# Performance work log

Hardware: AMD Instinct MI355X
Metric: run time of the kernel (lower is better)

Reference implementation:

```python
import jax, jax.numpy as jnp
import numpy as np

N_NODES = 25000
N_EDGES = 250000
DIM = 64
HEADS = 4
BN_EPS = 1e-5


def setup_inputs() -> dict:
    key = jax.random.key(0)
    ks = jax.random.split(key, 6)
    x = jax.random.normal(ks[0], (N_NODES, DIM), dtype=jnp.float32)
    edge_index = jax.random.randint(ks[1], (2, N_EDGES), 0, N_NODES)
    edge_attr = jax.random.normal(ks[2], (N_EDGES, DIM), dtype=jnp.float32)
    # learned params of GATGNN_AGAT_LAYER (xavier-ish scale)
    W = jax.random.normal(ks[3], (2 * DIM, HEADS * DIM), dtype=jnp.float32) * 0.05
    att = jax.random.normal(ks[4], (1, HEADS, 2 * DIM), dtype=jnp.float32) * 0.05
    bias = jnp.zeros((DIM,), dtype=jnp.float32)
    # BatchNorm1d(heads) in eval mode (running stats)
    bn_gamma = jnp.ones((HEADS,), dtype=jnp.float32)
    bn_beta = jnp.zeros((HEADS,), dtype=jnp.float32)
    bn_mean = jnp.zeros((HEADS,), dtype=jnp.float32)
    bn_var = jnp.ones((HEADS,), dtype=jnp.float32)
    return {"x": x, "edge_attr": edge_attr, "W": W, "att": att, "bias": bias,
            "bn_gamma": bn_gamma, "bn_beta": bn_beta, "bn_mean": bn_mean,
            "bn_var": bn_var, "edge_index": edge_index}


def reference(x, edge_attr, W, att, bias, bn_gamma, bn_beta, bn_mean, bn_var, edge_index):
    act = jax.nn.softplus  # act='softplus' in DSDCrystal
    # flow='target_to_source': i = edge_index[0] (aggregation index), j = edge_index[1]
    idx_i = edge_index[0]
    idx_j = edge_index[1]
    x_i = x[idx_i]                                   # [E, D] gather
    x_j = x[idx_j]                                   # [E, D] gather
    out_i = act(jnp.concatenate([x_i, edge_attr], axis=-1) @ W)  # [E, H*D]
    out_j = act(jnp.concatenate([x_j, edge_attr], axis=-1) @ W)  # [E, H*D]
    out_i = out_i.reshape(-1, HEADS, DIM)            # [E, H, D]
    out_j = out_j.reshape(-1, HEADS, DIM)
    # multi-head attention logits
    alpha = act(jnp.sum(jnp.concatenate([out_i, out_j], axis=-1) * att, axis=-1))  # [E, H]
    # BatchNorm1d(heads), eval mode
    alpha = act((alpha - bn_mean) / jnp.sqrt(bn_var + BN_EPS) * bn_gamma + bn_beta)
    # segment softmax over edges sharing the same target node i
    amax = jax.ops.segment_max(alpha, idx_i, num_segments=N_NODES)  # [N, H]
    e = jnp.exp(alpha - amax[idx_i])
    denom = jax.ops.segment_sum(e, idx_i, num_segments=N_NODES)[idx_i]  # [E, H]
    alpha = e / denom
    # weighted messages, scatter-add aggregation (dropout p=0.0 / eval)
    msg = out_j * alpha[:, :, None]                  # [E, H, D]
    aggr = jax.ops.segment_sum(msg, idx_i, num_segments=N_NODES)  # [N, H, D]
    # update: mean over heads + bias
    return aggr.mean(axis=1) + bias                  # [N, D]
```

## Files before the change

kernel.cpp:

```cpp
#include <hip/hip_runtime.h>
#include <hip/hip_bf16.h>
#include <math.h>

#define NN 25000
#define NE 250000
#define DD 64
#define HH 4
#define NGROUP (NE / 16)
#define NB 98

typedef __attribute__((ext_vector_type(8))) short bf16x8;
typedef __attribute__((ext_vector_type(4))) float f32x4;

#define WT_LD 136

__device__ __forceinline__ float softplus_f(float x) {
    return fmaxf(x, 0.0f) + __logf(1.0f + __expf(-fabsf(x)));
}

__device__ __forceinline__ unsigned short f2bf(float f) {
    __hip_bfloat16 h = __float2bfloat16(f);
    unsigned short u;
    __builtin_memcpy(&u, &h, 2);
    return u;
}

__device__ __forceinline__ float bf2f(unsigned short u) {
    return __uint_as_float(((unsigned int)u) << 16);
}

__device__ __forceinline__ void load8(const float* p, bf16x8& hi, bf16x8& lo) {
    float4 a = *(const float4*)p;
    float4 b = *(const float4*)(p + 4);
    float v[8] = {a.x, a.y, a.z, a.w, b.x, b.y, b.z, b.w};
#pragma unroll
    for (int i = 0; i < 8; ++i) {
        unsigned short h = f2bf(v[i]);
        hi[i] = (short)h;
        lo[i] = (short)f2bf(v[i] - bf2f(h));
    }
}

__global__ __launch_bounds__(512, 4)
void k_edge(const float* __restrict__ x, const float* __restrict__ ea,
            const float* __restrict__ W, const float* __restrict__ att,
            const float* __restrict__ bn_g, const float* __restrict__ bn_b,
            const float* __restrict__ bn_m, const float* __restrict__ bn_v,
            const int* __restrict__ eidx, const int* __restrict__ perm,
            unsigned short* __restrict__ outj,
            float* __restrict__ expa, float* __restrict__ denom)
{
    __shared__ unsigned short Wsh[256 * WT_LD];
    __shared__ float attI[256], attJ[256];

    const int tid = threadIdx.x;
    const int lane = tid & 63;
    const int q = lane >> 4;
    const int r = lane & 15;

    for (int idx = tid; idx < 32768; idx += 512) {
        int k = idx >> 8, n = idx & 255;
        Wsh[n * WT_LD + k] = f2bf(W[idx]);
    }
    if (tid < 256) {
        int c = tid;
        attI[c] = att[(c >> 6) * 128 + (c & 63)];
        attJ[c] = att[(c >> 6) * 128 + 64 + (c & 63)];
    }
    float bnsc[HH], bnsh[HH];
#pragma unroll
    for (int t = 0; t < HH; ++t) {
        float inv = rsqrtf(bn_v[t] + 1e-5f);
        bnsc[t] = bn_g[t] * inv;
        bnsh[t] = bn_b[t] - bn_m[t] * bn_g[t] * inv;
    }
    __syncthreads();

    const int gw = blockIdx.x * 8 + (tid >> 6);
    const int nw = gridDim.x * 8;

    for (int g = gw; g < NGROUP; g += nw) {
        const int e0 = g * 16;
        const int pe = perm[e0 + r];
        const int ei = eidx[pe];
        const int ej = eidx[NE + pe];
        const float* xi = x + (size_t)ei * DD;
        const float* xj = x + (size_t)ej * DD;
        const float* ev = ea + (size_t)pe * DD;

        bf16x8 Ahi[6], Alo[6];
        load8(xi + q * 8,      Ahi[0], Alo[0]);
        load8(xi + 32 + q * 8, Ahi[1], Alo[1]);
        load8(xj + q * 8,      Ahi[2], Alo[2]);
        load8(xj + 32 + q * 8, Ahi[3], Alo[3]);
        load8(ev + q * 8,      Ahi[4], Alo[4]);
        load8(ev + 32 + q * 8, Ahi[5], Alo[5]);

        float lg[4][4];
#pragma unroll
        for (int a = 0; a < 4; ++a)
#pragma unroll
            for (int b = 0; b < 4; ++b) lg[a][b] = 0.f;

#pragma unroll
        for (int nt = 0; nt < 4; ++nt) {
            f32x4 ai[4], aj[4];
#pragma unroll
            for (int h = 0; h < 4; ++h) {
                ai[h] = (f32x4){0.f, 0.f, 0.f, 0.f};
                aj[h] = (f32x4){0.f, 0.f, 0.f, 0.f};
            }
#pragma unroll
            for (int h = 0; h < 4; ++h) {
                const unsigned short* bp = &Wsh[((nt + 4 * h) * 16 + r) * WT_LD + q * 8];
#pragma unroll
                for (int kt = 0; kt < 4; ++kt) {
                    bf16x8 bf = *(const bf16x8*)(bp + kt * 32);
                    const int fi = (kt < 2) ? kt : kt + 2;
                    const int fj = kt + 2;
                    ai[h] = __builtin_amdgcn_mfma_f32_16x16x32_bf16(Ahi[fi], bf, ai[h], 0, 0, 0);
                    ai[h] = __builtin_amdgcn_mfma_f32_16x16x32_bf16(Alo[fi], bf, ai[h], 0, 0, 0);
                    aj[h] = __builtin_amdgcn_mfma_f32_16x16x32_bf16(Ahi[fj], bf, aj[h], 0, 0, 0);
                    aj[h] = __builtin_amdgcn_mfma_f32_16x16x32_bf16(Alo[fj], bf, aj[h], 0, 0, 0);
                }
            }
            const int dbase = nt * 16 + r;
#pragma unroll
            for (int reg = 0; reg < 4; ++reg) {
                ushort4 pk;
                unsigned short* pkp = (unsigned short*)&pk;
#pragma unroll
                for (int h = 0; h < 4; ++h) {
                    const int c = dbase + 64 * h;
                    float spi = softplus_f(ai[h][reg]);
                    float spj = softplus_f(aj[h][reg]);
                    lg[reg][h] += spi * attI[c] + spj * attJ[c];
                    pkp[h] = f2bf(spj);
                }
                const unsigned p = (unsigned)(e0 + q * 4 + reg);
                *(ushort4*)&outj[p * 256 + dbase * 4] = pk;
            }
        }

#pragma unroll
        for (int off = 1; off < 16; off <<= 1) {
#pragma unroll
            for (int a = 0; a < 4; ++a)
#pragma unroll
                for (int b = 0; b < 4; ++b)
                    lg[a][b] += __shfl_xor(lg[a][b], off, 64);
        }
        float exv[4][4];
#pragma unroll
        for (int reg = 0; reg < 4; ++reg)
#pragma unroll
            for (int h = 0; h < 4; ++h)
                exv[reg][h] = __expf(softplus_f(fmaf(lg[reg][h], bnsc[h], bnsh[h])));

        int iis[4];
#pragma unroll
        for (int reg = 0; reg < 4; ++reg)
            iis[reg] = __shfl(ei, q * 4 + reg, 16);

        if (r < 4) {
#pragma unroll
            for (int reg = 0; reg < 4; ++reg) {
                const int p = e0 + q * 4 + reg;
                expa[p * 4 + r] = exv[reg][r];
                atomicAdd(&denom[iis[reg] * 4 + r], exv[reg][r]);
            }
        }
    }
}

__global__ __launch_bounds__(256)
void k_hist(const int* __restrict__ eidx, int* __restrict__ cnt) {
    const int e = blockIdx.x * 256 + threadIdx.x;
    if (e < NE) atomicAdd(&cnt[eidx[e]], 1);
}

__global__ __launch_bounds__(256)
void k_scanA(const int* __restrict__ cnt, int* __restrict__ offs,
             int* __restrict__ bsum) {
    __shared__ int s[256];
    const int tid = threadIdx.x;
    const int i = blockIdx.x * 256 + tid;
    int v = (i < NN) ? cnt[i] : 0;
    s[tid] = v;
    __syncthreads();
#pragma unroll
    for (int off = 1; off < 256; off <<= 1) {
        int t = (tid >= off) ? s[tid - off] : 0;
        __syncthreads();
        s[tid] += t;
        __syncthreads();
    }
    if (i < NN) offs[i] = s[tid] - v;
    if (tid == 255) bsum[blockIdx.x] = s[255];
}

__global__ __launch_bounds__(128)
void k_scanB(const int* __restrict__ bsum, int* __restrict__ bbase) {
    __shared__ int s[128];
    const int tid = threadIdx.x;
    int v = (tid < NB) ? bsum[tid] : 0;
    s[tid] = v;
    __syncthreads();
#pragma unroll
    for (int off = 1; off < 128; off <<= 1) {
        int t = (tid >= off) ? s[tid - off] : 0;
        __syncthreads();
        s[tid] += t;
        __syncthreads();
    }
    if (tid < NB) bbase[tid] = s[tid] - v;
}

__global__ __launch_bounds__(256)
void k_scanC(int* __restrict__ offs, const int* __restrict__ bbase,
             int* __restrict__ cursor) {
    const int i = blockIdx.x * 256 + threadIdx.x;
    if (i < NN) {
        const int o = offs[i] + bbase[blockIdx.x];
        offs[i] = o;
        cursor[i] = o;
    }
    if (i == 0) offs[NN] = NE;
}

__global__ __launch_bounds__(256)
void k_place(const int* __restrict__ eidx, int* __restrict__ cursor,
             int* __restrict__ perm) {
    const int e = blockIdx.x * 256 + threadIdx.x;
    if (e < NE) {
        const int pos = atomicAdd(&cursor[eidx[e]], 1);
        perm[pos] = e;
    }
}

__global__ __launch_bounds__(256)
void k_aggr(const int* __restrict__ offs,
            const unsigned short* __restrict__ outj,
            const float* __restrict__ expa,
            const float* __restrict__ denom,
            const float* __restrict__ bias,
            float* __restrict__ out)
{
    const int n = blockIdx.x * 4 + (threadIdx.x >> 6);
    if (n >= NN) return;
    const int lane = threadIdx.x & 63;
    const int k0 = offs[n], k1 = offs[n + 1];
    const float4 dv = *(const float4*)&denom[n * 4];
    float num0 = 0.f, num1 = 0.f, num2 = 0.f, num3 = 0.f;
    for (int k = k0; k < k1; ++k) {
        const float4 ex = *(const float4*)&expa[k * 4];
        const ushort4 v = *(const ushort4*)&outj[((unsigned)k << 8) | (lane << 2)];
        num0 += ex.x * bf2f(v.x);
        num1 += ex.y * bf2f(v.y);
        num2 += ex.z * bf2f(v.z);
        num3 += ex.w * bf2f(v.w);
    }
    float r = 0.f;
    r += (dv.x > 0.f) ? num0 / dv.x : 0.f;
    r += (dv.y > 0.f) ? num1 / dv.y : 0.f;
    r += (dv.z > 0.f) ? num2 / dv.z : 0.f;
    r += (dv.w > 0.f) ? num3 / dv.w : 0.f;
    out[n * DD + lane] = 0.25f * r + bias[lane];
}

extern "C" void kernel_launch(void* const* d_in, const int* in_sizes, int n_in,
                              void* d_out, int out_size, void* d_ws, size_t ws_size,
                              hipStream_t stream)
{
    (void)in_sizes; (void)n_in; (void)out_size; (void)ws_size;
    const float* x    = (const float*)d_in[0];
    const float* ea   = (const float*)d_in[1];
    const float* W    = (const float*)d_in[2];
    const float* att  = (const float*)d_in[3];
    const float* bias = (const float*)d_in[4];
    const float* bn_g = (const float*)d_in[5];
    const float* bn_b = (const float*)d_in[6];
    const float* bn_m = (const float*)d_in[7];
    const float* bn_v = (const float*)d_in[8];
    const int*   eidx = (const int*)d_in[9];
    float* out = (float*)d_out;

    char* ws = (char*)d_ws;
    unsigned short* outj = (unsigned short*)ws;
    float* expa  = (float*)(ws + (size_t)NE * 512);
    float* denom = (float*)(ws + (size_t)NE * 512 + (size_t)NE * 16);
    int*   cnt    = (int*)(denom + (size_t)NN * 4);
    int*   offs   = cnt + NN;
    int*   cursor = offs + NN + 1;
    int*   perm   = cursor + NN;
    int*   bsum   = perm + NE;
    int*   bbase  = bsum + NB;

    hipMemsetAsync(denom, 0, (size_t)NN * 5 * sizeof(int), stream);

    k_hist <<<dim3((NE + 255) / 256), dim3(256), 0, stream>>>(eidx, cnt);
    k_scanA<<<dim3(NB), dim3(256), 0, stream>>>(cnt, offs, bsum);
    k_scanB<<<dim3(1), dim3(128), 0, stream>>>(bsum, bbase);
    k_scanC<<<dim3(NB), dim3(256), 0, stream>>>(offs, bbase, cursor);
    k_place<<<dim3((NE + 255) / 256), dim3(256), 0, stream>>>(eidx, cursor, perm);

    k_edge<<<dim3(512), dim3(512), 0, stream>>>(
        x, ea, W, att, bn_g, bn_b, bn_m, bn_v, eidx, perm, outj, expa, denom);

    k_aggr<<<dim3((NN + 3) / 4), dim3(256), 0, stream>>>(
        offs, outj, expa, denom, bias, out);
}
```

Baseline: 321.1 us.

## Precompute per-node x@W_top once and gather it in edge kernel

Splits the concatenated matmul into a per-node part and a per-edge part. A new kernel computes x@W[0:64] once for each of the 25k nodes. The edge kernel then only runs the edge_attr@W[64:128] MFMA once per edge and adds the gathered per-node results for i and j, which cuts edge MFMA work by about 4x. In exchange it adds a 25.6MB fp32 workspace write and scattered 1KB-per-edge gathers of that buffer, in place of the original 256B x gathers, plus one extra kernel launch.

```diff
diff --git a/kernel.cpp b/kernel.cpp
--- a/kernel.cpp
+++ b/kernel.cpp
@@ -7,12 +7,13 @@
 #define DD 64
 #define HH 4
 #define NGROUP (NE / 16)
+#define NGX ((NN + 15) / 16)
 #define NB 98
 
 typedef __attribute__((ext_vector_type(8))) short bf16x8;
 typedef __attribute__((ext_vector_type(4))) float f32x4;
 
-#define WT_LD 136
+#define WB_LD 72
 
 __device__ __forceinline__ float softplus_f(float x) {
     return fmaxf(x, 0.0f) + __logf(1.0f + __expf(-fabsf(x)));
@@ -42,25 +43,81 @@
 }
 
 __global__ __launch_bounds__(512, 4)
-void k_edge(const float* __restrict__ x, const float* __restrict__ ea,
-            const float* __restrict__ W, const float* __restrict__ att,
-            const float* __restrict__ bn_g, const float* __restrict__ bn_b,
-            const float* __restrict__ bn_m, const float* __restrict__ bn_v,
-            const int* __restrict__ eidx, const int* __restrict__ perm,
-            unsigned short* __restrict__ outj,
-            float* __restrict__ expa, float* __restrict__ denom)
+void k_xw(const float* __restrict__ x, const float* __restrict__ W,
+          float* __restrict__ xw)
 {
-    __shared__ unsigned short Wsh[256 * WT_LD];
-    __shared__ float attI[256], attJ[256];
-
+    __shared__ unsigned short Wsh[256 * WB_LD];
     const int tid = threadIdx.x;
     const int lane = tid & 63;
     const int q = lane >> 4;
     const int r = lane & 15;
 
-    for (int idx = tid; idx < 32768; idx += 512) {
+    for (int idx = tid; idx < 16384; idx += 512) {
         int k = idx >> 8, n = idx & 255;
-        Wsh[n * WT_LD + k] = f2bf(W[idx]);
+        Wsh[n * WB_LD + k] = f2bf(W[k * 256 + n]);
+    }
+    __syncthreads();
+
+    const int gw = blockIdx.x * 8 + (tid >> 6);
+    const int nw = gridDim.x * 8;
+
+    for (int g = gw; g < NGX; g += nw) {
+        const int node = g * 16 + r;
+        const int nd = (node < NN) ? node : (NN - 1);
+        const float* xp = x + (size_t)nd * DD;
+        bf16x8 Ahi[2], Alo[2];
+        load8(xp + q * 8,      Ahi[0], Alo[0]);
+        load8(xp + 32 + q * 8, Ahi[1], Alo[1]);
+
+#pragma unroll
+        for (int nt = 0; nt < 4; ++nt) {
+            f32x4 acc[4];
+#pragma unroll
+            for (int h = 0; h < 4; ++h) acc[h] = (f32x4){0.f, 0.f, 0.f, 0.f};
+#pragma unroll
+            for (int h = 0; h < 4; ++h) {
+                const unsigned short* bp = &Wsh[((nt + 4 * h) * 16 + r) * WB_LD + q * 8];
+#pragma unroll
+                for (int kt = 0; kt < 2; ++kt) {
+                    bf16x8 bf = *(const bf16x8*)(bp + kt * 32);
+                    acc[h] = __builtin_amdgcn_mfma_f32_16x16x32_bf16(Ahi[kt], bf, acc[h], 0, 0, 0);
+                    acc[h] = __builtin_amdgcn_mfma_f32_16x16x32_bf16(Alo[kt], bf, acc[h], 0, 0, 0);
+                }
+            }
+#pragma unroll
+            for (int reg = 0; reg < 4; ++reg) {
+                const int row = g * 16 + q * 4 + reg;
+                if (row < NN) {
+#pragma unroll
+                    for (int h = 0; h < 4; ++h)
+                        xw[(size_t)row * 256 + 64 * h + nt * 16 + r] = acc[h][reg];
+                }
+            }
+        }
+    }
+}
+
+__global__ __launch_bounds__(512, 4)
+void k_edge(const float* __restrict__ ea, const float* __restrict__ W,
+            const float* __restrict__ att,
+            const float* __restrict__ bn_g, const float* __restrict__ bn_b,
+            const float* __restrict__ bn_m, const float* __restrict__ bn_v,
+            const int* __restrict__ eidx, const int* __restrict__ perm,
+            const float* __restrict__ xw,
+            unsigned short* __restrict__ outj,
+            float* __restrict__ expa, float* __restrict__ denom)
+{
+    __shared__ unsigned short Wsh[256 * WB_LD];
+    __shared__ float attI[256], attJ[256];
+
+    const int tid = threadIdx.x;
+    const int lane = tid & 63;
+    const int q = lane >> 4;
+    const int r = lane & 15;
+
+    for (int idx = tid; idx < 16384; idx += 512) {
+        int k = idx >> 8, n = idx & 255;
+        Wsh[n * WB_LD + k] = f2bf(W[(64 + k) * 256 + n]);
     }
     if (tid < 256) {
         int c = tid;
@@ -84,17 +141,22 @@
         const int pe = perm[e0 + r];
         const int ei = eidx[pe];
         const int ej = eidx[NE + pe];
-        const float* xi = x + (size_t)ei * DD;
-        const float* xj = x + (size_t)ej * DD;
         const float* ev = ea + (size_t)pe * DD;
 
-        bf16x8 Ahi[6], Alo[6];
-        load8(xi + q * 8,      Ahi[0], Alo[0]);
-        load8(xi + 32 + q * 8, Ahi[1], Alo[1]);
-        load8(xj + q * 8,      Ahi[2], Alo[2]);
-        load8(xj + 32 + q * 8, Ahi[3], Alo[3]);
-        load8(ev + q * 8,      Ahi[4], Alo[4]);
-        load8(ev + 32 + q * 8, Ahi[5], Alo[5]);
+        bf16x8 Ahi[2], Alo[2];
+        load8(ev + q * 8,      Ahi[0], Alo[0]);
+        load8(ev + 32 + q * 8, Ahi[1], Alo[1]);
+
+        int ii[4];
+        const float* xwi[4];
+        const float* xwj[4];
+#pragma unroll
+        for (int reg = 0; reg < 4; ++reg) {
+            ii[reg] = __shfl(ei, q * 4 + reg, 16);
+            const int jjr = __shfl(ej, q * 4 + reg, 16);
+            xwi[reg] = xw + (size_t)ii[reg] * 256;
+            xwj[reg] = xw + (size_t)jjr * 256;
+        }
 
         float lg[4][4];
 #pragma unroll
@@ -104,41 +166,36 @@
 
 #pragma unroll
         for (int nt = 0; nt < 4; ++nt) {
-            f32x4 ai[4], aj[4];
+            f32x4 aeC[4];
+#pragma unroll
+            for (int h = 0; h < 4; ++h) aeC[h] = (f32x4){0.f, 0.f, 0.f, 0.f};
 #pragma unroll
             for (int h = 0; h < 4; ++h) {
-                ai[h] = (f32x4){0.f, 0.f, 0.f, 0.f};
-                aj[h] = (f32x4){0.f, 0.f, 0.f, 0.f};
-            }
-#pragma unroll
-            for (int h = 0; h < 4; ++h) {
-                const unsigned short* bp = &Wsh[((nt + 4 * h) * 16 + r) * WT_LD + q * 8];
-#pragma unroll
-                for (int kt = 0; kt < 4; ++kt) {
+                const unsigned short* bp = &Wsh[((nt + 4 * h) * 16 + r) * WB_LD + q * 8];
+#pragma unroll
+                for (int kt = 0; kt < 2; ++kt) {
                     bf16x8 bf = *(const bf16x8*)(bp + kt * 32);
-                    const int fi = (kt < 2) ? kt : kt + 2;
-                    const int fj = kt + 2;
-                    ai[h] = __builtin_amdgcn_mfma_f32_16x16x32_bf16(Ahi[fi], bf, ai[h], 0, 0, 0);
-                    ai[h] = __builtin_amdgcn_mfma_f32_16x16x32_bf16(Alo[fi], bf, ai[h], 0, 0, 0);
-                    aj[h] = __builtin_amdgcn_mfma_f32_16x16x32_bf16(Ahi[fj], bf, aj[h], 0, 0, 0);
-                    aj[h] = __builtin_amdgcn_mfma_f32_16x16x32_bf16(Alo[fj], bf, aj[h], 0, 0, 0);
+                    aeC[h] = __builtin_amdgcn_mfma_f32_16x16x32_bf16(Ahi[kt], bf, aeC[h], 0, 0, 0);
+                    aeC[h] = __builtin_amdgcn_mfma_f32_16x16x32_bf16(Alo[kt], bf, aeC[h], 0, 0, 0);
                 }
             }
-            const int dbase = nt * 16 + r;
+            const int cbase = nt * 16 + r;
 #pragma unroll
             for (int reg = 0; reg < 4; ++reg) {
                 ushort4 pk;
                 unsigned short* pkp = (unsigned short*)&pk;
 #pragma unroll
                 for (int h = 0; h < 4; ++h) {
-                    const int c = dbase + 64 * h;
-                    float spi = softplus_f(ai[h][reg]);
-                    float spj = softplus_f(aj[h][reg]);
+                    const int c = cbase + 64 * h;
+                    float ci = xwi[reg][c] + aeC[h][reg];
+                    float cj = xwj[reg][c] + aeC[h][reg];
+                    float spi = softplus_f(ci);
+                    float spj = softplus_f(cj);
                     lg[reg][h] += spi * attI[c] + spj * attJ[c];
                     pkp[h] = f2bf(spj);
                 }
                 const unsigned p = (unsigned)(e0 + q * 4 + reg);
-                *(ushort4*)&outj[p * 256 + dbase * 4] = pk;
+                *(ushort4*)&outj[p * 256 + cbase * 4] = pk;
             }
         }
 
@@ -156,18 +213,13 @@
 #pragma unroll
             for (int h = 0; h < 4; ++h)
                 exv[reg][h] = __expf(softplus_f(fmaf(lg[reg][h], bnsc[h], bnsh[h])));
-
-        int iis[4];
-#pragma unroll
-        for (int reg = 0; reg < 4; ++reg)
-            iis[reg] = __shfl(ei, q * 4 + reg, 16);
 
         if (r < 4) {
 #pragma unroll
             for (int reg = 0; reg < 4; ++reg) {
                 const int p = e0 + q * 4 + reg;
                 expa[p * 4 + r] = exv[reg][r];
-                atomicAdd(&denom[iis[reg] * 4 + r], exv[reg][r]);
+                atomicAdd(&denom[ii[reg] * 4 + r], exv[reg][r]);
             }
         }
     }
@@ -295,9 +347,11 @@
     int*   perm   = cursor + NN;
     int*   bsum   = perm + NE;
     int*   bbase  = bsum + NB;
+    float* xwbuf  = (float*)(bbase + NB + 2);
 
     hipMemsetAsync(denom, 0, (size_t)NN * 5 * sizeof(int), stream);
 
+    k_xw   <<<dim3((NGX + 7) / 8), dim3(512), 0, stream>>>(x, W, xwbuf);
     k_hist <<<dim3((NE + 255) / 256), dim3(256), 0, stream>>>(eidx, cnt);
     k_scanA<<<dim3(NB), dim3(256), 0, stream>>>(cnt, offs, bsum);
     k_scanB<<<dim3(1), dim3(128), 0, stream>>>(bsum, bbase);
@@ -305,7 +359,7 @@
     k_place<<<dim3((NE + 255) / 256), dim3(256), 0, stream>>>(eidx, cursor, perm);
 
     k_edge<<<dim3(512), dim3(512), 0, stream>>>(
-        x, ea, W, att, bn_g, bn_b, bn_m, bn_v, eidx, perm, outj, expa, denom);
+        ea, W, att, bn_g, bn_b, bn_m, bn_v, eidx, perm, xwbuf, outj, expa, denom);
 
     k_aggr<<<dim3((NN + 3) / 4), dim3(256), 0, stream>>>(
         offs, outj, expa, denom, bias, out);
```

Measured after the change: 364.8 us. 1.14x slower.

## Merge three-pass scan into single-block scan and double edge-kernel block size

Applied to the files above, without the earlier changes.

Replaces the three-kernel offset scan (block scan, block-sum scan, fixup) with one 1024-thread single-block kernel, where each thread scans 25 counts serially. This removes two kernel launches and their inter-kernel gaps. Separately, the edge kernel moves to 1024-thread blocks (16 waves) so each block's shared-memory W staging serves twice as many waves. The larger blocks risk register pressure under launch_bounds(1024,8) and lower occupancy, since each block still holds a ~70KB shared tile.

```diff
diff --git a/kernel.cpp b/kernel.cpp
--- a/kernel.cpp
+++ b/kernel.cpp
@@ -41,7 +41,7 @@
     }
 }
 
-__global__ __launch_bounds__(512, 4)
+__global__ __launch_bounds__(1024, 8)
 void k_edge(const float* __restrict__ x, const float* __restrict__ ea,
             const float* __restrict__ W, const float* __restrict__ att,
             const float* __restrict__ bn_g, const float* __restrict__ bn_b,
@@ -58,7 +58,7 @@
     const int q = lane >> 4;
     const int r = lane & 15;
 
-    for (int idx = tid; idx < 32768; idx += 512) {
+    for (int idx = tid; idx < 32768; idx += 1024) {
         int k = idx >> 8, n = idx & 255;
         Wsh[n * WT_LD + k] = f2bf(W[idx]);
     }
@@ -76,8 +76,8 @@
     }
     __syncthreads();
 
-    const int gw = blockIdx.x * 8 + (tid >> 6);
-    const int nw = gridDim.x * 8;
+    const int gw = blockIdx.x * 16 + (tid >> 6);
+    const int nw = gridDim.x * 16;
 
     for (int g = gw; g < NGROUP; g += nw) {
         const int e0 = g * 16;
@@ -179,53 +179,40 @@
     if (e < NE) atomicAdd(&cnt[eidx[e]], 1);
 }
 
-__global__ __launch_bounds__(256)
-void k_scanA(const int* __restrict__ cnt, int* __restrict__ offs,
-             int* __restrict__ bsum) {
-    __shared__ int s[256];
+__global__ __launch_bounds__(1024)
+void k_scan(const int* __restrict__ cnt, int* __restrict__ offs,
+            int* __restrict__ cursor) {
+    __shared__ int s[1024];
     const int tid = threadIdx.x;
-    const int i = blockIdx.x * 256 + tid;
-    int v = (i < NN) ? cnt[i] : 0;
-    s[tid] = v;
+    const int lo = tid * 25;
+    int loc[25];
+    int sum = 0;
+    if (lo < NN) {
+#pragma unroll
+        for (int i = 0; i < 25; ++i) {
+            loc[i] = cnt[lo + i];
+            sum += loc[i];
+        }
+    }
+    s[tid] = sum;
     __syncthreads();
 #pragma unroll
-    for (int off = 1; off < 256; off <<= 1) {
+    for (int off = 1; off < 1024; off <<= 1) {
         int t = (tid >= off) ? s[tid - off] : 0;
         __syncthreads();
         s[tid] += t;
         __syncthreads();
     }
-    if (i < NN) offs[i] = s[tid] - v;
-    if (tid == 255) bsum[blockIdx.x] = s[255];
-}
-
-__global__ __launch_bounds__(128)
-void k_scanB(const int* __restrict__ bsum, int* __restrict__ bbase) {
-    __shared__ int s[128];
-    const int tid = threadIdx.x;
-    int v = (tid < NB) ? bsum[tid] : 0;
-    s[tid] = v;
-    __syncthreads();
-#pragma unroll
-    for (int off = 1; off < 128; off <<= 1) {
-        int t = (tid >= off) ? s[tid - off] : 0;
-        __syncthreads();
-        s[tid] += t;
-        __syncthreads();
-    }
-    if (tid < NB) bbase[tid] = s[tid] - v;
-}
-
-__global__ __launch_bounds__(256)
-void k_scanC(int* __restrict__ offs, const int* __restrict__ bbase,
-             int* __restrict__ cursor) {
-    const int i = blockIdx.x * 256 + threadIdx.x;
-    if (i < NN) {
-        const int o = offs[i] + bbase[blockIdx.x];
-        offs[i] = o;
-        cursor[i] = o;
-    }
-    if (i == 0) offs[NN] = NE;
+    if (lo < NN) {
+        int running = s[tid] - sum;
+#pragma unroll
+        for (int i = 0; i < 25; ++i) {
+            offs[lo + i] = running;
+            cursor[lo + i] = running;
+            running += loc[i];
+        }
+    }
+    if (tid == 0) offs[NN] = NE;
 }
 
 __global__ __launch_bounds__(256)
@@ -293,18 +280,14 @@
     int*   offs   = cnt + NN;
     int*   cursor = offs + NN + 1;
     int*   perm   = cursor + NN;
-    int*   bsum   = perm + NE;
-    int*   bbase  = bsum + NB;
 
     hipMemsetAsync(denom, 0, (size_t)NN * 5 * sizeof(int), stream);
 
     k_hist <<<dim3((NE + 255) / 256), dim3(256), 0, stream>>>(eidx, cnt);
-    k_scanA<<<dim3(NB), dim3(256), 0, stream>>>(cnt, offs, bsum);
-    k_scanB<<<dim3(1), dim3(128), 0, stream>>>(bsum, bbase);
-    k_scanC<<<dim3(NB), dim3(256), 0, stream>>>(offs, bbase, cursor);
+    k_scan <<<dim3(1), dim3(1024), 0, stream>>>(cnt, offs, cursor);
     k_place<<<dim3((NE + 255) / 256), dim3(256), 0, stream>>>(eidx, cursor, perm);
 
-    k_edge<<<dim3(512), dim3(512), 0, stream>>>(
+    k_edge<<<dim3(512), dim3(1024), 0, stream>>>(
         x, ea, W, att, bn_g, bn_b, bn_m, bn_v, eidx, perm, outj, expa, denom);
 
     k_aggr<<<dim3((NN + 3) / 4), dim3(256), 0, stream>>>(
```

Measured after the change: 810.9 us. 2.53x slower.
